# Performance work log

Hardware: AMD Instinct MI355X
Metric: run time of the kernel (lower is better)

## Reference

```python
import jax, jax.numpy as jnp
import numpy as np

ODE_UNFOLDS = 6  # ncps LTC default ode unfolds per timestep
EPS = 1e-8
UNITS, MOTOR, SENSORY = 48, 4, 1283


def setup_inputs() -> dict:
    key = jax.random.key(0)
    ks = jax.random.split(key, 24)
    B, S, H, W = 32, 8, 128, 80
    u = lambda k, shape, lo, hi: jax.random.uniform(k, shape, jnp.float32, lo, hi)

    depth_image = jax.random.uniform(ks[0], (B, S, H, W), jnp.float32)
    relative_position = jax.random.normal(ks[1], (B, S, 3), jnp.float32)

    def conv_init(k, o, i):
        k1, k2 = jax.random.split(k)
        scale = 1.0 / np.sqrt(i * 9)
        return (jax.random.uniform(k1, (o, i, 3, 3), jnp.float32, -scale, scale),
                jax.random.uniform(k2, (o,), jnp.float32, -scale, scale))

    w1, b1 = conv_init(ks[2], 128, 1)
    w2, b2 = conv_init(ks[3], 64, 128)
    w3, b3 = conv_init(ks[4], 64, 64)
    w4, b4 = conv_init(ks[5], 32, 64)

    # LTC parameters, init ranges as in ncps library
    gleak = u(ks[6], (UNITS,), 0.001, 1.0)
    vleak = u(ks[7], (UNITS,), -0.2, 0.2)
    cm = u(ks[8], (UNITS,), 0.4, 0.6)
    mu = u(ks[9], (UNITS, UNITS), 0.3, 0.8)
    sigma = u(ks[10], (UNITS, UNITS), 3.0, 8.0)
    w_syn = u(ks[11], (UNITS, UNITS), 0.001, 1.0)
    erev = jnp.sign(jax.random.normal(ks[12], (UNITS, UNITS)))
    mask = (jax.random.uniform(ks[13], (UNITS, UNITS)) < 0.5).astype(jnp.float32)
    sensory_mu = u(ks[14], (SENSORY, UNITS), 0.3, 0.8)
    sensory_sigma = u(ks[15], (SENSORY, UNITS), 3.0, 8.0)
    sensory_w = u(ks[16], (SENSORY, UNITS), 0.001, 1.0)
    sensory_erev = jnp.sign(jax.random.normal(ks[17], (SENSORY, UNITS)))
    sensory_mask = (jax.random.uniform(ks[18], (SENSORY, UNITS)) < 0.25).astype(jnp.float32)
    input_w = jnp.ones((SENSORY,), jnp.float32)
    input_b = jnp.zeros((SENSORY,), jnp.float32)
    output_w = jnp.ones((MOTOR,), jnp.float32)
    output_b = jnp.zeros((MOTOR,), jnp.float32)
    head_w = u(ks[19], (MOTOR, 2), -0.5, 0.5)
    head_b = jnp.zeros((2,), jnp.float32)

    return dict(depth_image=depth_image, relative_position=relative_position,
                w1=w1, b1=b1, w2=w2, b2=b2, w3=w3, b3=b3, w4=w4, b4=b4,
                gleak=gleak, vleak=vleak, cm=cm, mu=mu, sigma=sigma, w_syn=w_syn,
                erev=erev, mask=mask, sensory_mu=sensory_mu, sensory_sigma=sensory_sigma,
                sensory_w=sensory_w, sensory_erev=sensory_erev, sensory_mask=sensory_mask,
                input_w=input_w, input_b=input_b, output_w=output_w, output_b=output_b,
                head_w=head_w, head_b=head_b)


def reference(depth_image, relative_position, w1, b1, w2, b2, w3, b3, w4, b4,
              gleak, vleak, cm, mu, sigma, w_syn, erev, mask,
              sensory_mu, sensory_sigma, sensory_w, sensory_erev, sensory_mask,
              input_w, input_b, output_w, output_b, head_w, head_b):
    B, S = depth_image.shape[:2]
    # ---- CNN over all B*S depth frames ----
    x = depth_image.reshape(B * S, 1, depth_image.shape[2], depth_image.shape[3])
    for wc, bc in ((w1, b1), (w2, b2), (w3, b3), (w4, b4)):
        x = jax.lax.conv_general_dilated(x, wc, (2, 2), [(1, 1), (1, 1)])
        x = jax.nn.relu(x + bc[None, :, None, None])
    feats = x.reshape(B, S, -1)                                   # [B,S,1280]
    feats = jnp.concatenate([feats, relative_position.reshape(B, S, -1)], axis=2)  # [B,S,1283]

    # ---- NCP LTC recurrence (ncps LTCCell math) ----
    inputs = feats * input_w + input_b
    cm_t = cm * ODE_UNFOLDS  # cm / (elapsed_time / ode_unfolds), elapsed_time = 1

    def step(v_pre, inp):  # inp: [B, 1283]
        sact = sensory_w * jax.nn.sigmoid(sensory_sigma * (inp[:, :, None] - sensory_mu)) * sensory_mask  # [B,1283,48]
        w_num_s = jnp.sum(sact * sensory_erev, axis=1)  # [B,48]
        w_den_s = jnp.sum(sact, axis=1)                 # [B,48]

        def unfold(v, _):
            act = w_syn * jax.nn.sigmoid(sigma * (v[:, :, None] - mu)) * mask  # [B,48,48]
            num = cm_t * v + gleak * vleak + jnp.sum(act * erev, axis=1) + w_num_s
            den = cm_t + gleak + jnp.sum(act, axis=1) + w_den_s
            return num / (den + EPS), None

        v_pre, _ = jax.lax.scan(unfold, v_pre, None, length=ODE_UNFOLDS)
        return v_pre, v_pre

    v0 = jnp.zeros((B, UNITS), depth_image.dtype)
    _, states = jax.lax.scan(step, v0, jnp.swapaxes(inputs, 0, 1))  # states: [S,B,48]
    outputs = states[:, :, :MOTOR] * output_w + output_b            # [S,B,4]
    out = jnp.mean(jnp.swapaxes(outputs, 0, 1), axis=1)             # [B,4]
    return jnp.tanh(out @ head_w + head_b)                          # [B,2]
```

## Files before the change

### kernel.cpp

```cpp
#include <hip/hip_runtime.h>
#include <math.h>


typedef __attribute__((ext_vector_type(8))) short short8v;
typedef __attribute__((ext_vector_type(16))) float float16v;

__device__ __forceinline__ unsigned short f2bf(float x) {
    unsigned int u = __float_as_uint(x);
    u = u + 0x7fffu + ((u >> 16) & 1u);
    return (unsigned short)(u >> 16);
}
__device__ __forceinline__ float bf2f(unsigned short b) {
    return __uint_as_float(((unsigned int)b) << 16);
}

__global__ __launch_bounds__(256) void k_prep_wB(const float* __restrict__ w2,
                                                 unsigned short* __restrict__ wB) {
    int idx = blockIdx.x * 256 + threadIdx.x;
    if (idx >= 294912) return;
    int j = idx & 7;
    int lane = (idx >> 3) & 63;
    int hl = (idx >> 9) & 1;
    int t = idx >> 10;
    int s = t % 9;
    int u = t / 9;
    int icb = u & 7;
    int Nt = u >> 3;
    int oc = Nt * 32 + (lane & 31);
    int ic = icb * 16 + 8 * (lane >> 5) + j;
    int kh = s / 3, kw = s % 3;
    float w = w2[((size_t)oc * 128 + ic) * 9 + kh * 3 + kw];
    unsigned short h = f2bf(w);
    wB[idx] = hl ? f2bf(w - bf2f(h)) : h;
}

__global__ void k_transpose_w(const float* __restrict__ src, float* __restrict__ dst,
                              int OC, int IC) {
    int idx = blockIdx.x * blockDim.x + threadIdx.x;
    int total = OC * IC * 9;
    if (idx >= total) return;
    int oc = idx / (IC * 9);
    int rem = idx % (IC * 9);
    int ic = rem / 9;
    int k = rem % 9;
    dst[(ic * 9 + k) * OC + oc] = src[idx];
}

__global__ __launch_bounds__(640) void k_conv12(
    const float* __restrict__ depth,
    const float* __restrict__ w1g, const float* __restrict__ b1g,
    const unsigned short* __restrict__ wB,
    const float* __restrict__ b2,
    float* __restrict__ out)
{
    __shared__ float lds_d[35 * 84];
    __shared__ unsigned short c1h[12512];
    __shared__ unsigned short c1l[12512];

    const int tid = threadIdx.x;
    const int lane = tid & 63;
    const int wv = __builtin_amdgcn_readfirstlane(tid >> 6);
    const int Nt = wv & 1;
    const int Mt = wv >> 1;
    const int n = blockIdx.x >> 2;
    const int q = blockIdx.x & 3;

    const float* dimg = depth + (size_t)n * 128 * 80;
    const int dr0 = 32 * q - 3;
    for (int idx = tid; idx < 35 * 82; idx += 640) {
        int rr = idx / 82, c = idx - rr * 82;
        int gr = dr0 + rr, gc = c - 1;
        float v = 0.f;
        if (gr >= 0 && gr < 128 && gc >= 0 && gc < 80) v = dimg[gr * 80 + gc];
        lds_d[rr * 84 + c] = v;
    }

    float16v acc = {0.f, 0.f, 0.f, 0.f, 0.f, 0.f, 0.f, 0.f,
                    0.f, 0.f, 0.f, 0.f, 0.f, 0.f, 0.f, 0.f};

    const int l31 = lane & 31;
    const int px = Mt * 32 + l31;
    const int oh = px / 20;
    const int ow = px - oh * 20;
    const int icblk = lane >> 5;
    const int baseA = icblk * 782 + oh * 46 + ow;

    for (int icb = 0; icb < 8; ++icb) {
        short8v Bh[9], Bl[9];
        const unsigned short* wchunk = wB + (size_t)(Nt * 8 + icb) * 9216 + lane * 8;
#pragma unroll
        for (int s = 0; s < 9; ++s) {
            Bh[s] = *(const short8v*)(wchunk + s * 1024);
            Bl[s] = *(const short8v*)(wchunk + s * 1024 + 512);
        }

        __syncthreads();
        for (int it = tid; it < 714; it += 640) {
            const int r = it / 42, C = it - r * 42;
            const int g = 16 * q - 1 + r;
            const int cc = C - 1;
            const int p = C & 1, cc2 = C >> 1;
            const bool valid = (g >= 0 && g < 64 && cc >= 0 && cc < 40);
            float d[3][3];
            if (valid) {
                const float* dp = &lds_d[(2 * r) * 84 + (2 * C - 2)];
#pragma unroll
                for (int kh2 = 0; kh2 < 3; ++kh2) {
                    float2 a = *(const float2*)&dp[kh2 * 84];
                    d[kh2][0] = a.x; d[kh2][1] = a.y; d[kh2][2] = dp[kh2 * 84 + 2];
                }
            }
#pragma unroll
            for (int icl = 0; icl < 16; icl += 2) {
                unsigned int hpack = 0, lpack = 0;
#pragma unroll
                for (int tt = 0; tt < 2; ++tt) {
                    float v = 0.f;
                    if (valid) {
                        const int ic = icb * 16 + icl + tt;
                        float sacc = b1g[ic];
#pragma unroll
                        for (int kh2 = 0; kh2 < 3; ++kh2)
#pragma unroll
                            for (int kw2 = 0; kw2 < 3; ++kw2)
                                sacc = fmaf(d[kh2][kw2], w1g[ic * 9 + kh2 * 3 + kw2], sacc);
                        v = fmaxf(sacc, 0.f);
                    }
                    unsigned short h = f2bf(v);
                    unsigned short l = f2bf(v - bf2f(h));
                    hpack |= ((unsigned int)h) << (16 * tt);
                    lpack |= ((unsigned int)l) << (16 * tt);
                }
                const int off = ((((icl >> 3) * 2 + p) * 17 + r) * 23 + cc2) * 8 + (icl & 7);
                *(unsigned int*)&c1h[off] = hpack;
                *(unsigned int*)&c1l[off] = lpack;
            }
        }
        __syncthreads();

#pragma unroll
        for (int s = 0; s < 9; ++s) {
            const int kh = s / 3, kw = s % 3;
            const int offe = (baseA + (kw & 1) * 391 + kh * 23 + (kw >> 1)) * 8;
            short8v Ah = *(const short8v*)&c1h[offe];
            short8v Al = *(const short8v*)&c1l[offe];
            acc = __builtin_amdgcn_mfma_f32_32x32x16_bf16(Ah, Bh[s], acc, 0, 0, 0);
            acc = __builtin_amdgcn_mfma_f32_32x32x16_bf16(Ah, Bl[s], acc, 0, 0, 0);
            acc = __builtin_amdgcn_mfma_f32_32x32x16_bf16(Al, Bh[s], acc, 0, 0, 0);
        }
    }

    const int oc = Nt * 32 + l31;
    const float bb = b2[oc];
    float* obase = out + ((size_t)n * 64 + oc) * 640;
#pragma unroll
    for (int qd = 0; qd < 4; ++qd) {
        const int px4 = q * 160 + Mt * 32 + 8 * qd + 4 * icblk;
        float4 v;
        v.x = fmaxf(acc[4 * qd + 0] + bb, 0.f);
        v.y = fmaxf(acc[4 * qd + 1] + bb, 0.f);
        v.z = fmaxf(acc[4 * qd + 2] + bb, 0.f);
        v.w = fmaxf(acc[4 * qd + 3] + bb, 0.f);
        *(float4*)&obase[px4] = v;
    }
}

__global__ __launch_bounds__(512, 2) void k_conv3(
    const float* __restrict__ in,
    const float* __restrict__ w3T,
    const float* __restrict__ bias,
    float* __restrict__ out)
{
    constexpr int IC = 64, IH = 32, IW = 20;
    constexpr int CR = 33, CC = 22, CCP = 26, ICB = 8;
    __shared__ float lds_in[ICB * CR * CCP];

    const int tid = threadIdx.x;
    const int lane = tid & 63;
    const int wv = tid >> 6;
    const int ocg16 = __builtin_amdgcn_readfirstlane(wv >> 1) * 16;
    const int half = __builtin_amdgcn_readfirstlane(wv & 1);
    const int n = blockIdx.x;
    const float* ibase = in + (size_t)n * IC * IH * IW;

    float acc[2][16];
#pragma unroll
    for (int p = 0; p < 2; ++p)
#pragma unroll
        for (int e = 0; e < 16; ++e) acc[p][e] = 0.f;

    const int oh_l = lane / 5, owp = lane - oh_l * 5;
    const int oh_g = half * 8 + oh_l;

    for (int icb = 0; icb < IC / ICB; ++icb) {
        const int ic0 = icb * ICB;
        __syncthreads();
        for (int idx = tid; idx < ICB * CR * CC; idx += 512) {
            int icl = idx / (CR * CC);
            int rem = idx - icl * (CR * CC);
            int r = rem / CC, c = rem - r * CC;
            int ih = r - 1, iw = c - 1;
            float v = 0.f;
            if (ih >= 0 && ih < IH && iw >= 0 && iw < IW)
                v = ibase[((size_t)(ic0 + icl) * IH + ih) * IW + iw];
            lds_in[(icl * CR + r) * CCP + c] = v;
        }
        __syncthreads();
        if (lane < 40) {
#pragma unroll
            for (int icl = 0; icl < ICB; ++icl) {
                float patch[3][5];
#pragma unroll
                for (int rr = 0; rr < 3; ++rr) {
                    const float* cp = &lds_in[(icl * CR + 2 * oh_g + rr) * CCP + 4 * owp];
                    float2 a = *(const float2*)&cp[0];
                    float2 b = *(const float2*)&cp[2];
                    patch[rr][0] = a.x; patch[rr][1] = a.y;
                    patch[rr][2] = b.x; patch[rr][3] = b.y;
                    patch[rr][4] = cp[4];
                }
                const float* __restrict__ wk = w3T + (size_t)(ic0 + icl) * 576 + ocg16;
#pragma unroll
                for (int k = 0; k < 9; ++k) {
                    const int kh = k / 3, kw = k - kh * 3;
#pragma unroll
                    for (int e = 0; e < 16; ++e) {
                        const float w = wk[k * 64 + e];
                        acc[0][e] = fmaf(patch[kh][kw], w, acc[0][e]);
                        acc[1][e] = fmaf(patch[kh][2 + kw], w, acc[1][e]);
                    }
                }
            }
        }
    }
    if (lane < 40) {
#pragma unroll
        for (int e = 0; e < 16; ++e) {
            const int oc = ocg16 + e;
            const float bb = bias[oc];
            float2 r0;
            r0.x = fmaxf(acc[0][e] + bb, 0.f);
            r0.y = fmaxf(acc[1][e] + bb, 0.f);
            *(float2*)&out[((size_t)n * 64 + oc) * 160 + oh_g * 10 + 2 * owp] = r0;
        }
    }
}

__global__ __launch_bounds__(256) void k_sens4(
    const float* __restrict__ conv3o,
    const float* __restrict__ w4, const float* __restrict__ b4,
    const float* __restrict__ relpos,
    const float* __restrict__ smu, const float* __restrict__ ssig,
    const float* __restrict__ sw, const float* __restrict__ sev,
    const float* __restrict__ smask,
    const float* __restrict__ iw, const float* __restrict__ ib,
    float* __restrict__ wns, float* __restrict__ wds)
{
    constexpr int CR = 17, CW = 12;
    constexpr int NS = 1283, U = 48, NG = 5;
    __shared__ float lds_in[64 * CR * CW];
    __shared__ float lds_inp[NS];
    __shared__ float lds_pn[NG * U], lds_pd[NG * U];

    const int tid = threadIdx.x;
    const int bs = blockIdx.x;
    const float* ibase = conv3o + (size_t)bs * 64 * 160;

    for (int idx = tid; idx < 64 * CR * CW; idx += 256) {
        int ic = idx / (CR * CW);
        int rem = idx - ic * (CR * CW);
        int r = rem / CW, c = rem - r * CW;
        int ih = r - 1, iww = c - 1;
        float v = 0.f;
        if (ih >= 0 && ih < 16 && iww >= 0 && iww < 10)
            v = ibase[ic * 160 + ih * 10 + iww];
        lds_in[idx] = v;
    }
    if (tid < 3) lds_inp[1280 + tid] = relpos[bs * 3 + tid] * iw[1280 + tid] + ib[1280 + tid];
    __syncthreads();

    const int oc = tid >> 3, pg = tid & 7;
    float acc5[5];
#pragma unroll
    for (int j = 0; j < 5; ++j) acc5[j] = 0.f;
    const float* wp = w4 + oc * 576;
    for (int ic = 0; ic < 64; ++ic) {
        float rv[3][12];
#pragma unroll
        for (int rr = 0; rr < 3; ++rr) {
            const float* rp = &lds_in[(ic * CR + 2 * pg + rr) * CW];
            float4 a = *(const float4*)&rp[0];
            float4 b = *(const float4*)&rp[4];
            float4 c = *(const float4*)&rp[8];
            rv[rr][0] = a.x; rv[rr][1] = a.y; rv[rr][2] = a.z; rv[rr][3] = a.w;
            rv[rr][4] = b.x; rv[rr][5] = b.y; rv[rr][6] = b.z; rv[rr][7] = b.w;
            rv[rr][8] = c.x; rv[rr][9] = c.y; rv[rr][10] = c.z; rv[rr][11] = c.w;
        }
        float wv[9];
#pragma unroll
        for (int k = 0; k < 9; ++k) wv[k] = wp[ic * 9 + k];
#pragma unroll
        for (int k = 0; k < 9; ++k) {
            const int kh = k / 3, kw = k - kh * 3;
#pragma unroll
            for (int j = 0; j < 5; ++j)
                acc5[j] = fmaf(rv[kh][2 * j + kw], wv[k], acc5[j]);
        }
    }
    const float bb = b4[oc];
#pragma unroll
    for (int j = 0; j < 5; ++j) {
        const int f = oc * 40 + pg * 5 + j;
        lds_inp[f] = fmaxf(acc5[j] + bb, 0.f) * iw[f] + ib[f];
    }
    __syncthreads();

    if (tid < NG * U) {
        const int p = tid / U, j = tid % U;
        const int i0 = (NS * p) / NG, i1 = (NS * (p + 1)) / NG;
        float pn = 0.f, pd = 0.f;
        for (int i = i0; i < i1; ++i) {
            float x = lds_inp[i];
            int o = i * U + j;
            float arg = ssig[o] * (x - smu[o]);
            float e = __expf(-arg);
            float r = 1.f / (1.f + e);
            float sact = sw[o] * r * smask[o];
            pn = fmaf(sact, sev[o], pn);
            pd += sact;
        }
        lds_pn[tid] = pn;
        lds_pd[tid] = pd;
    }
    __syncthreads();
    if (tid < U) {
        float sn = 0.f, sd = 0.f;
#pragma unroll
        for (int p = 0; p < NG; ++p) { sn += lds_pn[p * U + tid]; sd += lds_pd[p * U + tid]; }
        wns[bs * U + tid] = sn;
        wds[bs * U + tid] = sd;
    }
}

__global__ __launch_bounds__(192) void k_recur(
    const float* __restrict__ wns, const float* __restrict__ wds,
    const float* __restrict__ gleak, const float* __restrict__ vleak,
    const float* __restrict__ cm,
    const float* __restrict__ mu, const float* __restrict__ sigma,
    const float* __restrict__ wsyn, const float* __restrict__ erev,
    const float* __restrict__ mask,
    const float* __restrict__ ow_, const float* __restrict__ ob_,
    const float* __restrict__ hw, const float* __restrict__ hb,
    float* __restrict__ outp)
{
    constexpr int U = 48, S = 8, NU = 6, P = 4;
    constexpr float LOG2E = 1.44269504088896f;
    __shared__ float A[U * U], Bc[U * U], WE[U * U], WM[U * U];
    __shared__ float vv[U];
    __shared__ float pn[P * U], pd[P * U];
    __shared__ float out4[4];

    const int tid = threadIdx.x;
    const int b = blockIdx.x;
    const int p = tid / U, j = tid % U;

    for (int idx = tid; idx < U * U; idx += 192) {
        float sg = sigma[idx], m = mu[idx], w = wsyn[idx] * mask[idx];
        A[idx] = -sg * LOG2E;
        Bc[idx] = sg * m * LOG2E;
        WE[idx] = w * erev[idx];
        WM[idx] = w;
    }
    if (tid < U) vv[tid] = 0.f;
    float cmt = 0.f, gl = 0.f, glvl = 0.f;
    if (tid < U) {
        cmt = cm[tid] * 6.f;
        gl = gleak[tid];
        glvl = gl * vleak[tid];
    }
    float acc_o = 0.f;
    __syncthreads();

    for (int s = 0; s < S; ++s) {
        float wn = 0.f, wd = 0.f;
        if (tid < U) {
            wn = wns[(b * S + s) * U + tid];
            wd = wds[(b * S + s) * U + tid];
        }
        for (int u = 0; u < NU; ++u) {
            float an = 0.f, ad = 0.f;
            const int i0 = p * 12;
#pragma unroll
            for (int ii = 0; ii < 12; ++ii) {
                int i = i0 + ii;
                float vi = vv[i];
                int o = i * U + j;
                float e = exp2f(fmaf(vi, A[o], Bc[o]));
                float r = 1.f / (1.f + e);
                an = fmaf(WE[o], r, an);
                ad = fmaf(WM[o], r, ad);
            }
            pn[tid] = an;
            pd[tid] = ad;
            __syncthreads();
            if (tid < U) {
                float num = fmaf(cmt, vv[tid], glvl) + wn;
                float den = cmt + gl + wd;
#pragma unroll
                for (int qq = 0; qq < P; ++qq) { num += pn[qq * U + tid]; den += pd[qq * U + tid]; }
                vv[tid] = num / (den + 1e-8f);
            }
            __syncthreads();
        }
        if (tid < 4) acc_o += vv[tid];
    }
    if (tid < 4) out4[tid] = (acc_o * 0.125f) * ow_[tid] + ob_[tid];
    __syncthreads();
    if (tid < 2) {
        float r = hb[tid];
#pragma unroll
        for (int k = 0; k < 4; ++k) r += out4[k] * hw[k * 2 + tid];
        outp[b * 2 + tid] = tanhf(r);
    }
}

extern "C" void kernel_launch(void* const* d_in, const int* in_sizes, int n_in,
                              void* d_out, int out_size, void* d_ws, size_t ws_size,
                              hipStream_t stream) {
    const float* depth  = (const float*)d_in[0];
    const float* relpos = (const float*)d_in[1];
    const float* w1 = (const float*)d_in[2];
    const float* b1 = (const float*)d_in[3];
    const float* w2 = (const float*)d_in[4];
    const float* b2 = (const float*)d_in[5];
    const float* w3 = (const float*)d_in[6];
    const float* b3 = (const float*)d_in[7];
    const float* w4 = (const float*)d_in[8];
    const float* b4 = (const float*)d_in[9];
    const float* gleak = (const float*)d_in[10];
    const float* vleak = (const float*)d_in[11];
    const float* cm    = (const float*)d_in[12];
    const float* mu    = (const float*)d_in[13];
    const float* sigma = (const float*)d_in[14];
    const float* wsyn  = (const float*)d_in[15];
    const float* erev  = (const float*)d_in[16];
    const float* mask  = (const float*)d_in[17];
    const float* smu   = (const float*)d_in[18];
    const float* ssig  = (const float*)d_in[19];
    const float* sw    = (const float*)d_in[20];
    const float* sev   = (const float*)d_in[21];
    const float* smask = (const float*)d_in[22];
    const float* iw    = (const float*)d_in[23];
    const float* ib    = (const float*)d_in[24];
    const float* ow_   = (const float*)d_in[25];
    const float* ob_   = (const float*)d_in[26];
    const float* hw    = (const float*)d_in[27];
    const float* hb    = (const float*)d_in[28];

    float* ws = (float*)d_ws;
    float* conv2o = ws;
    float* conv3o = conv2o + 10485760;
    float* w3T    = conv3o + 2621440;
    float* wBf    = w3T + 36864;
    float* wnsb   = wBf + 147456;
    float* wdsb   = wnsb + 12288;
    unsigned short* wB = (unsigned short*)wBf;

    k_prep_wB<<<dim3(1152), dim3(256), 0, stream>>>(w2, wB);
    k_transpose_w<<<dim3((36864 + 255) / 256), dim3(256), 0, stream>>>(w3, w3T, 64, 64);

    k_conv12<<<dim3(1024), dim3(640), 0, stream>>>(depth, w1, b1, wB, b2, conv2o);
    k_conv3<<<dim3(256), dim3(512), 0, stream>>>(conv2o, w3T, b3, conv3o);
    k_sens4<<<dim3(256), dim3(256), 0, stream>>>(conv3o, w4, b4, relpos,
                                                 smu, ssig, sw, sev, smask,
                                                 iw, ib, wnsb, wdsb);
    k_recur<<<dim3(32), dim3(192), 0, stream>>>(wnsb, wdsb, gleak, vleak, cm, mu, sigma,
                                                wsyn, erev, mask, ow_, ob_, hw, hb,
                                                (float*)d_out);
}
```

Before: 581.2 us.

## Move conv3 to split-bf16 MFMA with NHWC bf16 hi/lo intermediate

Conv3 is rewritten from scalar FP32 FMAs to 32x32x16 bf16 MFMA using a hi/lo split (three products) so it keeps close to FP32 accuracy. Conv12 now writes its output as channel-last bf16 hi and lo halves instead of NCHW float, which gives conv3 contiguous 8-channel vector loads straight from global memory with no LDS staging. The weight-prep kernel is generalised so it also packs conv3 weights. The cost is scattered 2-byte stores in the conv12 epilogue and slightly lower precision from dropping the lo*lo term.

```diff
diff --git a/kernel.cpp b/kernel.cpp
--- a/kernel.cpp
+++ b/kernel.cpp
@@ -14,36 +14,25 @@
     return __uint_as_float(((unsigned int)b) << 16);
 }
 
-__global__ __launch_bounds__(256) void k_prep_wB(const float* __restrict__ w2,
-                                                 unsigned short* __restrict__ wB) {
+__global__ __launch_bounds__(256) void k_prep_w(const float* __restrict__ src,
+                                                unsigned short* __restrict__ dst,
+                                                int NICB, int IC, int total) {
     int idx = blockIdx.x * 256 + threadIdx.x;
-    if (idx >= 294912) return;
+    if (idx >= total) return;
     int j = idx & 7;
     int lane = (idx >> 3) & 63;
     int hl = (idx >> 9) & 1;
     int t = idx >> 10;
     int s = t % 9;
     int u = t / 9;
-    int icb = u & 7;
-    int Nt = u >> 3;
+    int icb = u % NICB;
+    int Nt = u / NICB;
     int oc = Nt * 32 + (lane & 31);
     int ic = icb * 16 + 8 * (lane >> 5) + j;
     int kh = s / 3, kw = s % 3;
-    float w = w2[((size_t)oc * 128 + ic) * 9 + kh * 3 + kw];
+    float w = src[((size_t)oc * IC + ic) * 9 + kh * 3 + kw];
     unsigned short h = f2bf(w);
-    wB[idx] = hl ? f2bf(w - bf2f(h)) : h;
-}
-
-__global__ void k_transpose_w(const float* __restrict__ src, float* __restrict__ dst,
-                              int OC, int IC) {
-    int idx = blockIdx.x * blockDim.x + threadIdx.x;
-    int total = OC * IC * 9;
-    if (idx >= total) return;
-    int oc = idx / (IC * 9);
-    int rem = idx % (IC * 9);
-    int ic = rem / 9;
-    int k = rem % 9;
-    dst[(ic * 9 + k) * OC + oc] = src[idx];
+    dst[idx] = hl ? f2bf(w - bf2f(h)) : h;
 }
 
 __global__ __launch_bounds__(640) void k_conv12(
@@ -51,7 +40,8 @@
     const float* __restrict__ w1g, const float* __restrict__ b1g,
     const unsigned short* __restrict__ wB,
     const float* __restrict__ b2,
-    float* __restrict__ out)
+    unsigned short* __restrict__ c2h,
+    unsigned short* __restrict__ c2l)
 {
     __shared__ float lds_d[35 * 84];
     __shared__ unsigned short c1h[12512];
@@ -152,97 +142,83 @@
 
     const int oc = Nt * 32 + l31;
     const float bb = b2[oc];
-    float* obase = out + ((size_t)n * 64 + oc) * 640;
 #pragma unroll
     for (int qd = 0; qd < 4; ++qd) {
-        const int px4 = q * 160 + Mt * 32 + 8 * qd + 4 * icblk;
+#pragma unroll
+        for (int t = 0; t < 4; ++t) {
+            const int pxg = q * 160 + Mt * 32 + 8 * qd + 4 * icblk + t;
+            float v = fmaxf(acc[4 * qd + t] + bb, 0.f);
+            unsigned short h = f2bf(v);
+            unsigned short l = f2bf(v - bf2f(h));
+            const size_t off = ((size_t)n * 640 + pxg) * 64 + oc;
+            c2h[off] = h;
+            c2l[off] = l;
+        }
+    }
+}
+
+__global__ __launch_bounds__(640) void k_conv3(
+    const unsigned short* __restrict__ c2h,
+    const unsigned short* __restrict__ c2l,
+    const unsigned short* __restrict__ wB3,
+    const float* __restrict__ bias,
+    float* __restrict__ out)
+{
+    const int tid = threadIdx.x;
+    const int lane = tid & 63;
+    const int wv = __builtin_amdgcn_readfirstlane(tid >> 6);
+    const int Nt = wv & 1;
+    const int Mt = wv >> 1;
+    const int n = blockIdx.x;
+    const int l31 = lane & 31;
+    const int icblk = lane >> 5;
+    const int px = Mt * 32 + l31;
+    const int oh = px / 10, ow = px - oh * 10;
+
+    float16v acc = {0.f, 0.f, 0.f, 0.f, 0.f, 0.f, 0.f, 0.f,
+                    0.f, 0.f, 0.f, 0.f, 0.f, 0.f, 0.f, 0.f};
+    const size_t fbase = (size_t)n * 640 * 64;
+
+    for (int icb = 0; icb < 4; ++icb) {
+        short8v Bh[9], Bl[9];
+        const unsigned short* wchunk = wB3 + (size_t)(Nt * 4 + icb) * 9216 + lane * 8;
+#pragma unroll
+        for (int s = 0; s < 9; ++s) {
+            Bh[s] = *(const short8v*)(wchunk + s * 1024);
+            Bl[s] = *(const short8v*)(wchunk + s * 1024 + 512);
+        }
+        const int icoff = icb * 16 + icblk * 8;
+#pragma unroll
+        for (int s = 0; s < 9; ++s) {
+            const int kh = s / 3, kw = s % 3;
+            const int row = 2 * oh - 1 + kh;
+            const int col = 2 * ow - 1 + kw;
+            const bool valid = ((unsigned)row < 32u) && ((unsigned)col < 20u);
+            short8v Ah = {0, 0, 0, 0, 0, 0, 0, 0};
+            short8v Al = {0, 0, 0, 0, 0, 0, 0, 0};
+            if (valid) {
+                const size_t off = fbase + ((size_t)(row * 20 + col)) * 64 + icoff;
+                Ah = *(const short8v*)(c2h + off);
+                Al = *(const short8v*)(c2l + off);
+            }
+            acc = __builtin_amdgcn_mfma_f32_32x32x16_bf16(Ah, Bh[s], acc, 0, 0, 0);
+            acc = __builtin_amdgcn_mfma_f32_32x32x16_bf16(Ah, Bl[s], acc, 0, 0, 0);
+            acc = __builtin_amdgcn_mfma_f32_32x32x16_bf16(Al, Bh[s], acc, 0, 0, 0);
+        }
+    }
+
+    const int oc = Nt * 32 + l31;
+    const float bb = bias[oc];
+    float* obase = out + ((size_t)n * 64 + oc) * 160;
+#pragma unroll
+    for (int qd = 0; qd < 4; ++qd) {
+        const int px4 = Mt * 32 + 8 * qd + 4 * icblk;
         float4 v;
         v.x = fmaxf(acc[4 * qd + 0] + bb, 0.f);
         v.y = fmaxf(acc[4 * qd + 1] + bb, 0.f);
         v.z = fmaxf(acc[4 * qd + 2] + bb, 0.f);
         v.w = fmaxf(acc[4 * qd + 3] + bb, 0.f);
         *(float4*)&obase[px4] = v;
-    }
-}
-
-__global__ __launch_bounds__(512, 2) void k_conv3(
-    const float* __restrict__ in,
-    const float* __restrict__ w3T,
-    const float* __restrict__ bias,
-    float* __restrict__ out)
-{
-    constexpr int IC = 64, IH = 32, IW = 20;
-    constexpr int CR = 33, CC = 22, CCP = 26, ICB = 8;
-    __shared__ float lds_in[ICB * CR * CCP];
-
-    const int tid = threadIdx.x;
-    const int lane = tid & 63;
-    const int wv = tid >> 6;
-    const int ocg16 = __builtin_amdgcn_readfirstlane(wv >> 1) * 16;
-    const int half = __builtin_amdgcn_readfirstlane(wv & 1);
-    const int n = blockIdx.x;
-    const float* ibase = in + (size_t)n * IC * IH * IW;
-
-    float acc[2][16];
-#pragma unroll
-    for (int p = 0; p < 2; ++p)
-#pragma unroll
-        for (int e = 0; e < 16; ++e) acc[p][e] = 0.f;
-
-    const int oh_l = lane / 5, owp = lane - oh_l * 5;
-    const int oh_g = half * 8 + oh_l;
-
-    for (int icb = 0; icb < IC / ICB; ++icb) {
-        const int ic0 = icb * ICB;
-        __syncthreads();
-        for (int idx = tid; idx < ICB * CR * CC; idx += 512) {
-            int icl = idx / (CR * CC);
-            int rem = idx - icl * (CR * CC);
-            int r = rem / CC, c = rem - r * CC;
-            int ih = r - 1, iw = c - 1;
-            float v = 0.f;
-            if (ih >= 0 && ih < IH && iw >= 0 && iw < IW)
-                v = ibase[((size_t)(ic0 + icl) * IH + ih) * IW + iw];
-            lds_in[(icl * CR + r) * CCP + c] = v;
-        }
-        __syncthreads();
-        if (lane < 40) {
-#pragma unroll
-            for (int icl = 0; icl < ICB; ++icl) {
-                float patch[3][5];
-#pragma unroll
-                for (int rr = 0; rr < 3; ++rr) {
-                    const float* cp = &lds_in[(icl * CR + 2 * oh_g + rr) * CCP + 4 * owp];
-                    float2 a = *(const float2*)&cp[0];
-                    float2 b = *(const float2*)&cp[2];
-                    patch[rr][0] = a.x; patch[rr][1] = a.y;
-                    patch[rr][2] = b.x; patch[rr][3] = b.y;
-                    patch[rr][4] = cp[4];
-                }
-                const float* __restrict__ wk = w3T + (size_t)(ic0 + icl) * 576 + ocg16;
-#pragma unroll
-                for (int k = 0; k < 9; ++k) {
-                    const int kh = k / 3, kw = k - kh * 3;
-#pragma unroll
-                    for (int e = 0; e < 16; ++e) {
-                        const float w = wk[k * 64 + e];
-                        acc[0][e] = fmaf(patch[kh][kw], w, acc[0][e]);
-                        acc[1][e] = fmaf(patch[kh][2 + kw], w, acc[1][e]);
-                    }
-                }
-            }
-        }
-    }
-    if (lane < 40) {
-#pragma unroll
-        for (int e = 0; e < 16; ++e) {
-            const int oc = ocg16 + e;
-            const float bb = bias[oc];
-            float2 r0;
-            r0.x = fmaxf(acc[0][e] + bb, 0.f);
-            r0.y = fmaxf(acc[1][e] + bb, 0.f);
-            *(float2*)&out[((size_t)n * 64 + oc) * 160 + oh_g * 10 + 2 * owp] = r0;
-        }
     }
 }
 
@@ -457,20 +433,19 @@
     const float* hw    = (const float*)d_in[27];
     const float* hb    = (const float*)d_in[28];
 
-    float* ws = (float*)d_ws;
-    float* conv2o = ws;
-    float* conv3o = conv2o + 10485760;
-    float* w3T    = conv3o + 2621440;
-    float* wBf    = w3T + 36864;
-    float* wnsb   = wBf + 147456;
+    unsigned short* c2h = (unsigned short*)d_ws;
+    unsigned short* c2l = c2h + 10485760;
+    unsigned short* wB  = c2l + 10485760;
+    unsigned short* wB3 = wB + 294912;
+    float* conv3o = (float*)(wB3 + 147456);
+    float* wnsb   = conv3o + 2621440;
     float* wdsb   = wnsb + 12288;
-    unsigned short* wB = (unsigned short*)wBf;
-
-    k_prep_wB<<<dim3(1152), dim3(256), 0, stream>>>(w2, wB);
-    k_transpose_w<<<dim3((36864 + 255) / 256), dim3(256), 0, stream>>>(w3, w3T, 64, 64);
-
-    k_conv12<<<dim3(1024), dim3(640), 0, stream>>>(depth, w1, b1, wB, b2, conv2o);
-    k_conv3<<<dim3(256), dim3(512), 0, stream>>>(conv2o, w3T, b3, conv3o);
+
+    k_prep_w<<<dim3(1152), dim3(256), 0, stream>>>(w2, wB, 8, 128, 294912);
+    k_prep_w<<<dim3(576), dim3(256), 0, stream>>>(w3, wB3, 4, 64, 147456);
+
+    k_conv12<<<dim3(1024), dim3(640), 0, stream>>>(depth, w1, b1, wB, b2, c2h, c2l);
+    k_conv3<<<dim3(256), dim3(640), 0, stream>>>(c2h, c2l, wB3, b3, conv3o);
     k_sens4<<<dim3(256), dim3(256), 0, stream>>>(conv3o, w4, b4, relpos,
                                                  smu, ssig, sw, sev, smask,
                                                  iw, ib, wnsb, wdsb);
```

After: 515.4 us. 11.3% less time.
